# Kernel optimization log

Measured on AMD Instinct MI355X. Metric: run time of the kernel, lower is better.

Reference implementation:

```python
import jax, jax.numpy as jnp
import numpy as np

B, K, D = 8192, 32, 256

def setup_inputs() -> dict:
    key = jax.random.key(0)
    ks = jax.random.split(key, 8)
    embedded_state = jax.random.normal(ks[0], (B, 1, D), dtype=jnp.float32)
    eps = jax.random.normal(ks[1], (B, 1, D), dtype=jnp.float32)
    W_mu = 0.02 * jax.random.normal(ks[2], (D, D), dtype=jnp.float32)
    b_mu = jnp.zeros((D,), dtype=jnp.float32)
    W_sig = 0.02 * jax.random.normal(ks[3], (D, D), dtype=jnp.float32)
    b_sig = jnp.zeros((D,), dtype=jnp.float32)
    mu_c = jax.random.uniform(ks[4], (K, D), dtype=jnp.float32)
    log_sigma_sq_c = jnp.zeros((K, D), dtype=jnp.float32)
    return {"embedded_state": embedded_state, "eps": eps, "W_mu": W_mu, "b_mu": b_mu,
            "W_sig": W_sig, "b_sig": b_sig, "mu_c": mu_c, "log_sigma_sq_c": log_sigma_sq_c}

def reference(embedded_state, eps, W_mu, b_mu, W_sig, b_sig, mu_c, log_sigma_sq_c):
    # linear projections (torch Linear: x @ W.T + b)
    mu_z = jnp.einsum('bnd,ed->bne', embedded_state, W_mu) + b_mu          # [B,1,D]
    log_sigma_sq_z = jnp.einsum('bnd,ed->bne', embedded_state, W_sig) + b_sig  # [B,1,D]
    z = mu_z + jnp.sqrt(jnp.exp(log_sigma_sq_z)) * eps                      # [B,1,D]
    inv_sig_c = jnp.exp(-log_sigma_sq_c)                                    # [K,D]
    # cluster-distance logits: broadcast [B,1,D] vs [K,D] -> [B,K,D] -> sum D
    pi_logits = -jnp.sum((z - mu_c[None]) ** 2 * inv_sig_c[None], axis=-1)  # [B,K]
    pi_post = jax.nn.softmax(pi_logits, axis=-1) + 1e-10                    # [B,K]
    # GMM loss terms (original code implicitly broadcasts pi_post over D)
    a = log_sigma_sq_c[None] + jnp.exp(log_sigma_sq_z) * inv_sig_c[None]    # [B,K,D]
    b = (mu_z - mu_c[None]) ** 2 * inv_sig_c[None]                          # [B,K,D]
    c = a + b
    batch_gaussian_loss = 0.5 * jnp.sum(pi_post[:, :, None] * c)
    mean_pi = jnp.mean(pi_post, axis=0)                                     # [K]
    batch_uniform_loss = jnp.mean(mean_pi * jnp.log(mean_pi))
    return z, batch_gaussian_loss, batch_uniform_loss
```

## Files before the change

kernel.cpp:

```cpp
#include <hip/hip_runtime.h>
#include <hip/hip_bf16.h>

typedef __attribute__((ext_vector_type(4))) float f32x4;
typedef __attribute__((ext_vector_type(8))) short short8;

#define NB 8192
#define ND 256
#define NK 32
#define PADF 520

static __device__ __forceinline__ unsigned short f2bf(float f) {
  return __builtin_bit_cast(unsigned short, __float2bfloat16(f));
}

static __device__ __forceinline__ f32x4 mfma_bf16(short8 a, short8 b, f32x4 c) {
  return __builtin_amdgcn_mfma_f32_16x16x32_bf16(a, b, c, 0, 0, 0);
}

static __device__ __forceinline__ short8 pack_bf16x8(float4 lo, float4 hi) {
  short8 r;
  r[0] = (short)f2bf(lo.x); r[1] = (short)f2bf(lo.y);
  r[2] = (short)f2bf(lo.z); r[3] = (short)f2bf(lo.w);
  r[4] = (short)f2bf(hi.x); r[5] = (short)f2bf(hi.y);
  r[6] = (short)f2bf(hi.z); r[7] = (short)f2bf(hi.w);
  return r;
}

__global__ __launch_bounds__(256) void prep_k(const float* __restrict__ wmu,
                                              const float* __restrict__ wsig,
                                              __hip_bfloat16* __restrict__ wsw,
                                              const float* __restrict__ mu_c,
                                              const float* __restrict__ lsc,
                                              __hip_bfloat16* __restrict__ bcsw,
                                              float* __restrict__ c3k,
                                              float* __restrict__ ckk) {
  __shared__ float red1[4], red2[4];
  const int blk = blockIdx.x, tid = threadIdx.x;
  if (blk < 512) {
    int i = blk * 256 + tid;
    int f = i >> 9, r = i & 511;
    int l = r >> 3, e = r & 7;
    int n = (f >> 3) * 16 + (l & 15);
    int k = (f & 7) * 32 + ((l >> 4) << 3) + e;
    float v = (n < 256) ? wmu[n * ND + k] : wsig[(n - 256) * ND + k];
    wsw[i] = __float2bfloat16(v);
  } else {
    int k = blk - 512;
    int d = tid;
    float l = lsc[k * ND + d];
    float inv = __expf(-l);
    float mc = mu_c[k * ND + d];
    const int rb = k >> 4, lrow = k & 15;
    {
      int c = d;
      int kb = c >> 5, q = (c >> 3) & 3, e = c & 7;
      bcsw[(size_t)(rb * 16 + kb) * 512 + (q * 16 + lrow) * 8 + e] = __float2bfloat16(inv);
    }
    {
      int c = 256 + d;
      int kb = c >> 5, q = (c >> 3) & 3, e = c & 7;
      bcsw[(size_t)(rb * 16 + kb) * 512 + (q * 16 + lrow) * 8 + e] = __float2bfloat16(-2.f * mc * inv);
    }
    float s1 = l, s2 = mc * mc * inv;
    #pragma unroll
    for (int sh = 32; sh; sh >>= 1) { s1 += __shfl_xor(s1, sh); s2 += __shfl_xor(s2, sh); }
    int lane = tid & 63, wv = tid >> 6;
    if (lane == 0) { red1[wv] = s1; red2[wv] = s2; }
    __syncthreads();
    if (tid == 0) {
      float t1 = red1[0] + red1[1] + red1[2] + red1[3];
      float t2 = red2[0] + red2[1] + red2[2] + red2[3];
      c3k[k] = t2;
      ckk[k] = t1 + t2;
    }
  }
}

__global__ __launch_bounds__(512, 4) void mega_k(const float* __restrict__ xf,
                                                 const __hip_bfloat16* __restrict__ wsw,
                                                 const float* __restrict__ bmu,
                                                 const float* __restrict__ bsigv,
                                                 const float* __restrict__ eps,
                                                 const __hip_bfloat16* __restrict__ bcsw,
                                                 const float* __restrict__ c3k,
                                                 const float* __restrict__ ckk,
                                                 float* __restrict__ zout,
                                                 float* __restrict__ part) {
  __shared__ __align__(16) unsigned short AcT[16][PADF];
  __shared__ __align__(16) unsigned short AqT[16][PADF];
  __shared__ __align__(16) char uniBuf[33792];
  __shared__ float piP[NK];
  __shared__ float gSum;
  unsigned short (*Axb)[264] = (unsigned short (*)[264])uniBuf;
  float (*sW)[2][16][33] = (float (*)[2][16][33])uniBuf;

  const int tid = threadIdx.x, lane = tid & 63, w = tid >> 6;
  const int lrow = lane & 15, q = lane >> 4;
  const int m0 = blockIdx.x * 16;

  if (tid < NK) piP[tid] = 0.f;
  if (tid == NK) gSum = 0.f;

  float bmv[2], bsv[2], epv[2][4];
  #pragma unroll
  for (int r = 0; r < 2; ++r) {
    const int d = (r * 8 + w) * 16 + lrow;
    bmv[r] = bmu[d];
    bsv[r] = bsigv[d];
    #pragma unroll
    for (int j = 0; j < 4; ++j)
      epv[r][j] = eps[(size_t)(m0 + q * 4 + j) * ND + d];
  }

  {
    const int r = tid >> 5, c0 = (tid & 31) * 8;
    const float* xr = xf + (size_t)(m0 + r) * ND + c0;
    float4 a0 = *reinterpret_cast<const float4*>(xr);
    float4 a1 = *reinterpret_cast<const float4*>(xr + 4);
    *reinterpret_cast<short8*>(&Axb[r][c0]) = pack_bf16x8(a0, a1);
  }
  __syncthreads();

  short8 aF[8];
  #pragma unroll
  for (int kk = 0; kk < 8; ++kk)
    aF[kk] = *reinterpret_cast<const short8*>(&Axb[lrow][kk * 32 + q * 8]);

  #pragma unroll
  for (int r = 0; r < 2; ++r) {
    const int rb = r * 8 + w;
    const __hip_bfloat16* pM = wsw + (size_t)(rb * 8) * 512 + lane * 8;
    const __hip_bfloat16* pS = wsw + (size_t)((16 + rb) * 8) * 512 + lane * 8;
    f32x4 aM = (f32x4){0.f, 0.f, 0.f, 0.f};
    f32x4 aS = (f32x4){0.f, 0.f, 0.f, 0.f};
    {
      short8 bM[8];
      #pragma unroll
      for (int kk = 0; kk < 8; ++kk)
        bM[kk] = *reinterpret_cast<const short8*>(pM + kk * 512);
      #pragma unroll
      for (int kk = 0; kk < 8; ++kk)
        aM = mfma_bf16(aF[kk], bM[kk], aM);
    }
    {
      short8 bS[8];
      #pragma unroll
      for (int kk = 0; kk < 8; ++kk)
        bS[kk] = *reinterpret_cast<const short8*>(pS + kk * 512);
      #pragma unroll
      for (int kk = 0; kk < 8; ++kk)
        aS = mfma_bf16(aF[kk], bS[kk], aS);
    }
    const int d = rb * 16 + lrow;
    #pragma unroll
    for (int j = 0; j < 4; ++j) {
      const int bl = q * 4 + j;
      const int b = m0 + bl;
      float muv = aM[j] + bmv[r];
      float lsv = aS[j] + bsv[r];
      float sq  = __expf(lsv);
      float zv  = muv + sqrtf(sq) * epv[r][j];
      zout[(size_t)b * ND + d] = zv;
      AcT[bl][d]       = f2bf(zv * zv);
      AcT[bl][256 + d] = f2bf(zv);
      AqT[bl][d]       = f2bf(sq + muv * muv);
      AqT[bl][256 + d] = f2bf(muv);
    }
  }
  __syncthreads();

  f32x4 cL[2], cQ[2];
  cL[0] = cL[1] = cQ[0] = cQ[1] = (f32x4){0.f, 0.f, 0.f, 0.f};
  {
    short8 b0v[2], b1v[2], acv[2], aqv[2];
    #pragma unroll
    for (int ks = 0; ks < 2; ++ks) {
      const int kb = w * 2 + ks;
      b0v[ks] = *reinterpret_cast<const short8*>(bcsw + (size_t)kb * 512 + lane * 8);
      b1v[ks] = *reinterpret_cast<const short8*>(bcsw + (size_t)(16 + kb) * 512 + lane * 8);
      const int kc = kb * 32 + q * 8;
      acv[ks] = *reinterpret_cast<const short8*>(&AcT[lrow][kc]);
      aqv[ks] = *reinterpret_cast<const short8*>(&AqT[lrow][kc]);
    }
    #pragma unroll
    for (int ks = 0; ks < 2; ++ks) {
      cL[0] = mfma_bf16(acv[ks], b0v[ks], cL[0]);
      cL[1] = mfma_bf16(acv[ks], b1v[ks], cL[1]);
      cQ[0] = mfma_bf16(aqv[ks], b0v[ks], cQ[0]);
      cQ[1] = mfma_bf16(aqv[ks], b1v[ks], cQ[1]);
    }
  }
  #pragma unroll
  for (int nfk = 0; nfk < 2; ++nfk)
    #pragma unroll
    for (int j = 0; j < 4; ++j) {
      sW[w][0][q * 4 + j][nfk * 16 + lrow] = cL[nfk][j];
      sW[w][1][q * 4 + j][nfk * 16 + lrow] = cQ[nfk][j];
    }
  __syncthreads();

  if (tid < 256) {
    const int b = tid >> 4, kk = tid & 15;
    float L0 = 0.f, L1 = 0.f, Q0 = 0.f, Q1 = 0.f;
    #pragma unroll
    for (int ww = 0; ww < 8; ++ww) {
      L0 += sW[ww][0][b][kk];      L1 += sW[ww][0][b][kk + 16];
      Q0 += sW[ww][1][b][kk];      Q1 += sW[ww][1][b][kk + 16];
    }
    float l0 = -(L0 + c3k[kk]);
    float l1 = -(L1 + c3k[kk + 16]);
    float mx = fmaxf(l0, l1);
    #pragma unroll
    for (int s = 8; s; s >>= 1) mx = fmaxf(mx, __shfl_xor(mx, s));
    float p0 = __expf(l0 - mx), p1 = __expf(l1 - mx);
    float ps = p0 + p1;
    #pragma unroll
    for (int s = 8; s; s >>= 1) ps += __shfl_xor(ps, s);
    float pi0 = p0 / ps + 1e-10f;
    float pi1 = p1 / ps + 1e-10f;
    float g = pi0 * (Q0 + ckk[kk]) + pi1 * (Q1 + ckk[kk + 16]);
    #pragma unroll
    for (int s = 8; s; s >>= 1) g += __shfl_xor(g, s);
    atomicAdd(&piP[kk], pi0);
    atomicAdd(&piP[kk + 16], pi1);
    if (kk == 0) atomicAdd(&gSum, g);
  }
  __syncthreads();
  if (tid < NK)  part[(size_t)tid * 512 + blockIdx.x] = piP[tid];
  if (tid == NK) part[(size_t)NK * 512 + blockIdx.x] = 0.5f * gSum;
}

__global__ __launch_bounds__(256) void final_k(const float* __restrict__ part,
                                               float* __restrict__ out) {
  __shared__ double red[4][33];
  const int tid = threadIdx.x, lane = tid & 63, wv = tid >> 6;
  if (lane < 33) {
    const float4* p4 = reinterpret_cast<const float4*>(part + (size_t)lane * 512);
    double acc = 0.0;
    for (int i = wv * 32; i < wv * 32 + 32; ++i) {
      float4 v = p4[i];
      acc += (double)v.x + (double)v.y + (double)v.z + (double)v.w;
    }
    red[wv][lane] = acc;
  }
  __syncthreads();
  if (tid >= 64) return;
  double s = (tid < 33) ? (red[0][tid] + red[1][tid] + red[2][tid] + red[3][tid]) : 0.0;
  if (tid == 32) out[NB * ND] = (float)s;
  double t = 0.0;
  if (tid < 32) { double mk = s / (double)NB; t = mk * log(mk); }
  #pragma unroll
  for (int sh = 16; sh; sh >>= 1) t += __shfl_xor(t, sh);
  if (tid == 0) out[NB * ND + 1] = (float)(t / (double)NK);
}

extern "C" void kernel_launch(void* const* d_in, const int* in_sizes, int n_in,
                              void* d_out, int out_size, void* d_ws, size_t ws_size,
                              hipStream_t stream) {
  const float* x    = (const float*)d_in[0];
  const float* eps  = (const float*)d_in[1];
  const float* wmu  = (const float*)d_in[2];
  const float* bmu  = (const float*)d_in[3];
  const float* wsig = (const float*)d_in[4];
  const float* bsig = (const float*)d_in[5];
  const float* mu_c = (const float*)d_in[6];
  const float* lsc  = (const float*)d_in[7];
  float* out = (float*)d_out;

  char* ws = (char*)d_ws;
  __hip_bfloat16* wsw  = (__hip_bfloat16*)ws;
  __hip_bfloat16* bcsw = (__hip_bfloat16*)(ws + (256u << 10));
  float* c3k  = (float*)(ws + (288u << 10));
  float* ckk  = (float*)(ws + (288u << 10) + 256u);
  float* part = (float*)(ws + (288u << 10) + 512u);

  prep_k<<<544, 256, 0, stream>>>(wmu, wsig, wsw, mu_c, lsc, bcsw, c3k, ckk);
  mega_k<<<512, 512, 0, stream>>>(x, wsw, bmu, bsig, eps, bcsw, c3k, ckk, out, part);
  final_k<<<1, 256, 0, stream>>>(part, out);
}
```

Before: 26.18 us.

## Replace partial-sum buffer with global atomics and load A fragments directly

Each block now atomically adds its 33 per-cluster and loss partials into a small global accumulator, which prep_k zeroes. The final kernel shrinks to a single wave that reads 33 values instead of reducing a 33x512 partial array in double precision. Separately, the input row tile is loaded straight from global memory into bf16 MFMA fragments, which removes the LDS staging buffer and a __syncthreads. The trade-offs are float atomic contention across 512 blocks, a nondeterministic float summation order instead of the double-precision reduction, and less coalesced global loads for the x tile.

```diff
diff --git a/kernel.cpp b/kernel.cpp
--- a/kernel.cpp
+++ b/kernel.cpp
@@ -33,7 +33,8 @@
                                               const float* __restrict__ lsc,
                                               __hip_bfloat16* __restrict__ bcsw,
                                               float* __restrict__ c3k,
-                                              float* __restrict__ ckk) {
+                                              float* __restrict__ ckk,
+                                              float* __restrict__ g33) {
   __shared__ float red1[4], red2[4];
   const int blk = blockIdx.x, tid = threadIdx.x;
   if (blk < 512) {
@@ -47,6 +48,7 @@
   } else {
     int k = blk - 512;
     int d = tid;
+    if (blk == 543 && tid >= 128 && tid < 161) g33[tid - 128] = 0.f;
     float l = lsc[k * ND + d];
     float inv = __expf(-l);
     float mc = mu_c[k * ND + d];
@@ -85,14 +87,12 @@
                                                  const float* __restrict__ c3k,
                                                  const float* __restrict__ ckk,
                                                  float* __restrict__ zout,
-                                                 float* __restrict__ part) {
+                                                 float* __restrict__ g33) {
   __shared__ __align__(16) unsigned short AcT[16][PADF];
   __shared__ __align__(16) unsigned short AqT[16][PADF];
-  __shared__ __align__(16) char uniBuf[33792];
+  __shared__ float sW[8][2][16][33];
   __shared__ float piP[NK];
   __shared__ float gSum;
-  unsigned short (*Axb)[264] = (unsigned short (*)[264])uniBuf;
-  float (*sW)[2][16][33] = (float (*)[2][16][33])uniBuf;
 
   const int tid = threadIdx.x, lane = tid & 63, w = tid >> 6;
   const int lrow = lane & 15, q = lane >> 4;
@@ -112,19 +112,16 @@
       epv[r][j] = eps[(size_t)(m0 + q * 4 + j) * ND + d];
   }
 
+  short8 aF[8];
   {
-    const int r = tid >> 5, c0 = (tid & 31) * 8;
-    const float* xr = xf + (size_t)(m0 + r) * ND + c0;
-    float4 a0 = *reinterpret_cast<const float4*>(xr);
-    float4 a1 = *reinterpret_cast<const float4*>(xr + 4);
-    *reinterpret_cast<short8*>(&Axb[r][c0]) = pack_bf16x8(a0, a1);
-  }
-  __syncthreads();
-
-  short8 aF[8];
-  #pragma unroll
-  for (int kk = 0; kk < 8; ++kk)
-    aF[kk] = *reinterpret_cast<const short8*>(&Axb[lrow][kk * 32 + q * 8]);
+    const float* xr = xf + (size_t)(m0 + lrow) * ND + q * 8;
+    #pragma unroll
+    for (int kk = 0; kk < 8; ++kk) {
+      float4 lo = *reinterpret_cast<const float4*>(xr + kk * 32);
+      float4 hi = *reinterpret_cast<const float4*>(xr + kk * 32 + 4);
+      aF[kk] = pack_bf16x8(lo, hi);
+    }
+  }
 
   #pragma unroll
   for (int r = 0; r < 2; ++r) {
@@ -226,32 +223,23 @@
     if (kk == 0) atomicAdd(&gSum, g);
   }
   __syncthreads();
-  if (tid < NK)  part[(size_t)tid * 512 + blockIdx.x] = piP[tid];
-  if (tid == NK) part[(size_t)NK * 512 + blockIdx.x] = 0.5f * gSum;
-}
-
-__global__ __launch_bounds__(256) void final_k(const float* __restrict__ part,
-                                               float* __restrict__ out) {
-  __shared__ double red[4][33];
-  const int tid = threadIdx.x, lane = tid & 63, wv = tid >> 6;
-  if (lane < 33) {
-    const float4* p4 = reinterpret_cast<const float4*>(part + (size_t)lane * 512);
-    double acc = 0.0;
-    for (int i = wv * 32; i < wv * 32 + 32; ++i) {
-      float4 v = p4[i];
-      acc += (double)v.x + (double)v.y + (double)v.z + (double)v.w;
-    }
-    red[wv][lane] = acc;
-  }
-  __syncthreads();
-  if (tid >= 64) return;
-  double s = (tid < 33) ? (red[0][tid] + red[1][tid] + red[2][tid] + red[3][tid]) : 0.0;
-  if (tid == 32) out[NB * ND] = (float)s;
+  if (tid < NK)  atomicAdd(&g33[tid], piP[tid]);
+  if (tid == NK) atomicAdd(&g33[NK], 0.5f * gSum);
+}
+
+__global__ void final_k(const float* __restrict__ g33, float* __restrict__ out) {
+  int lane = threadIdx.x;
   double t = 0.0;
-  if (tid < 32) { double mk = s / (double)NB; t = mk * log(mk); }
+  if (lane < 32) {
+    double mk = (double)g33[lane] / (double)NB;
+    t = mk * log(mk);
+  }
   #pragma unroll
   for (int sh = 16; sh; sh >>= 1) t += __shfl_xor(t, sh);
-  if (tid == 0) out[NB * ND + 1] = (float)(t / (double)NK);
+  if (lane == 0) {
+    out[NB * ND]     = g33[32];
+    out[NB * ND + 1] = (float)(t / (double)NK);
+  }
 }
 
 extern "C" void kernel_launch(void* const* d_in, const int* in_sizes, int n_in,
@@ -272,9 +260,9 @@
   __hip_bfloat16* bcsw = (__hip_bfloat16*)(ws + (256u << 10));
   float* c3k  = (float*)(ws + (288u << 10));
   float* ckk  = (float*)(ws + (288u << 10) + 256u);
-  float* part = (float*)(ws + (288u << 10) + 512u);
-
-  prep_k<<<544, 256, 0, stream>>>(wmu, wsig, wsw, mu_c, lsc, bcsw, c3k, ckk);
-  mega_k<<<512, 512, 0, stream>>>(x, wsw, bmu, bsig, eps, bcsw, c3k, ckk, out, part);
-  final_k<<<1, 256, 0, stream>>>(part, out);
-}
+  float* g33  = (float*)(ws + (288u << 10) + 512u);
+
+  prep_k<<<544, 256, 0, stream>>>(wmu, wsig, wsw, mu_c, lsc, bcsw, c3k, ckk, g33);
+  mega_k<<<512, 512, 0, stream>>>(x, wsw, bmu, bsig, eps, bcsw, c3k, ckk, out, g33);
+  final_k<<<1, 64, 0, stream>>>(g33, out);
+}
```

Measured after the change: 36.58 us. 1.4x slower.

## Fuse final reduction into main kernel via atomics and last-block pattern

Applied to the files above, without the earlier changes.

Drops the separate single-block final reduction kernel. Each main block now atomically adds its per-cluster pi sums and loss partial into 8 replicated global accumulators. The last block, found with an atomic counter, computes the final scalars. This removes one kernel launch and the partials round-trip, at the cost of float atomics, which make the summation order nondeterministic and replace the double-precision accumulation with float.

```diff
diff --git a/kernel.cpp b/kernel.cpp
--- a/kernel.cpp
+++ b/kernel.cpp
@@ -33,7 +33,9 @@
                                               const float* __restrict__ lsc,
                                               __hip_bfloat16* __restrict__ bcsw,
                                               float* __restrict__ c3k,
-                                              float* __restrict__ ckk) {
+                                              float* __restrict__ ckk,
+                                              float* __restrict__ g33r,
+                                              int* __restrict__ cnt) {
   __shared__ float red1[4], red2[4];
   const int blk = blockIdx.x, tid = threadIdx.x;
   if (blk < 512) {
@@ -44,6 +46,10 @@
     int k = (f & 7) * 32 + ((l >> 4) << 3) + e;
     float v = (n < 256) ? wmu[n * ND + k] : wsig[(n - 256) * ND + k];
     wsw[i] = __float2bfloat16(v);
+  } else if (blk == 544) {
+    g33r[tid] = 0.f;
+    g33r[256 + tid] = 0.f;
+    if (tid == 0) *cnt = 0;
   } else {
     int k = blk - 512;
     int d = tid;
@@ -85,12 +91,14 @@
                                                  const float* __restrict__ c3k,
                                                  const float* __restrict__ ckk,
                                                  float* __restrict__ zout,
-                                                 float* __restrict__ part) {
+                                                 float* __restrict__ g33r,
+                                                 int* __restrict__ cnt) {
   __shared__ __align__(16) unsigned short AcT[16][PADF];
   __shared__ __align__(16) unsigned short AqT[16][PADF];
   __shared__ __align__(16) char uniBuf[33792];
   __shared__ float piP[NK];
   __shared__ float gSum;
+  __shared__ int lastB;
   unsigned short (*Axb)[264] = (unsigned short (*)[264])uniBuf;
   float (*sW)[2][16][33] = (float (*)[2][16][33])uniBuf;
 
@@ -226,32 +234,41 @@
     if (kk == 0) atomicAdd(&gSum, g);
   }
   __syncthreads();
-  if (tid < NK)  part[(size_t)tid * 512 + blockIdx.x] = piP[tid];
-  if (tid == NK) part[(size_t)NK * 512 + blockIdx.x] = 0.5f * gSum;
-}
-
-__global__ __launch_bounds__(256) void final_k(const float* __restrict__ part,
-                                               float* __restrict__ out) {
-  __shared__ double red[4][33];
-  const int tid = threadIdx.x, lane = tid & 63, wv = tid >> 6;
-  if (lane < 33) {
-    const float4* p4 = reinterpret_cast<const float4*>(part + (size_t)lane * 512);
-    double acc = 0.0;
-    for (int i = wv * 32; i < wv * 32 + 32; ++i) {
-      float4 v = p4[i];
-      acc += (double)v.x + (double)v.y + (double)v.z + (double)v.w;
-    }
-    red[wv][lane] = acc;
-  }
-  __syncthreads();
-  if (tid >= 64) return;
-  double s = (tid < 33) ? (red[0][tid] + red[1][tid] + red[2][tid] + red[3][tid]) : 0.0;
-  if (tid == 32) out[NB * ND] = (float)s;
-  double t = 0.0;
-  if (tid < 32) { double mk = s / (double)NB; t = mk * log(mk); }
-  #pragma unroll
-  for (int sh = 16; sh; sh >>= 1) t += __shfl_xor(t, sh);
-  if (tid == 0) out[NB * ND + 1] = (float)(t / (double)NK);
+
+  {
+    const int rpl = (blockIdx.x & 7) * 64;
+    if (tid < NK)
+      __hip_atomic_fetch_add(&g33r[rpl + tid], piP[tid],
+                             __ATOMIC_RELAXED, __HIP_MEMORY_SCOPE_AGENT);
+    if (tid == NK)
+      __hip_atomic_fetch_add(&g33r[rpl + NK], 0.5f * gSum,
+                             __ATOMIC_RELAXED, __HIP_MEMORY_SCOPE_AGENT);
+  }
+  __syncthreads();
+  if (tid == 0) {
+    int old = __hip_atomic_fetch_add(cnt, 1, __ATOMIC_ACQ_REL, __HIP_MEMORY_SCOPE_AGENT);
+    lastB = (old == (int)gridDim.x - 1);
+  }
+  __syncthreads();
+  if (!lastB) return;
+
+  if (tid < 33) {
+    float s = 0.f;
+    #pragma unroll
+    for (int rpl = 0; rpl < 8; ++rpl)
+      s += __hip_atomic_load(&g33r[rpl * 64 + tid], __ATOMIC_RELAXED,
+                             __HIP_MEMORY_SCOPE_AGENT);
+    float t = 0.f;
+    if (tid == 32) {
+      zout[NB * ND] = s;
+    } else {
+      float mk = s / (float)NB;
+      t = mk * __logf(mk);
+    }
+    #pragma unroll
+    for (int sh = 16; sh; sh >>= 1) t += __shfl_xor(t, sh);
+    if (tid == 0) zout[NB * ND + 1] = t / (float)NK;
+  }
 }
 
 extern "C" void kernel_launch(void* const* d_in, const int* in_sizes, int n_in,
@@ -272,9 +289,9 @@
   __hip_bfloat16* bcsw = (__hip_bfloat16*)(ws + (256u << 10));
   float* c3k  = (float*)(ws + (288u << 10));
   float* ckk  = (float*)(ws + (288u << 10) + 256u);
-  float* part = (float*)(ws + (288u << 10) + 512u);
-
-  prep_k<<<544, 256, 0, stream>>>(wmu, wsig, wsw, mu_c, lsc, bcsw, c3k, ckk);
-  mega_k<<<512, 512, 0, stream>>>(x, wsw, bmu, bsig, eps, bcsw, c3k, ckk, out, part);
-  final_k<<<1, 256, 0, stream>>>(part, out);
-}
+  float* g33r = (float*)(ws + (288u << 10) + 512u);
+  int*   cnt  = (int*)(ws + (288u << 10) + 512u + 2048u);
+
+  prep_k<<<545, 256, 0, stream>>>(wmu, wsig, wsw, mu_c, lsc, bcsw, c3k, ckk, g33r, cnt);
+  mega_k<<<512, 512, 0, stream>>>(x, wsw, bmu, bsig, eps, bcsw, c3k, ckk, out, g33r, cnt);
+}
```

After: 32.37 us. 23.7% more time.
